# Kernel tuning notes

Measured on AMD Instinct MI355X. Metric: run time of the kernel, lower is better.

The kernel has to match this reference:

```python
import jax, jax.numpy as jnp
import numpy as np

OUTPUT_DIM = 8192
LEAF_DIM = 128
FEAT = 1024
BATCH = 8192
NUM_LEAVES = int(np.ceil(OUTPUT_DIM / LEAF_DIM))          # 64
NUM_INTERNAL = NUM_LEAVES - 1                              # 63
DEPTH = int(np.ceil(np.log2(NUM_LEAVES)))                  # 6


def _build_path_maps():
    # Exactly mirrors the Keras layer's __init__ path-map construction.
    nodes = np.full((NUM_LEAVES, DEPTH), -1, dtype=np.int32)
    dirs_ = np.full((NUM_LEAVES, DEPTH), -1, dtype=np.int32)
    for leaf_idx in range(NUM_LEAVES):
        curr = NUM_INTERNAL + leaf_idx
        path, dirs = [], []
        while curr > 0:
            parent = (curr - 1) // 2
            path.append(parent)
            dirs.append((curr - 1) % 2)
            curr = parent
        n = len(path)
        nodes[leaf_idx, :n] = path[::-1]
        dirs_[leaf_idx, :n] = dirs[::-1]
    return jnp.asarray(nodes), jnp.asarray(dirs_)


def setup_inputs() -> dict:
    key = jax.random.key(0)
    k1, k2, k3 = jax.random.split(key, 3)
    x = jax.random.normal(k1, (BATCH, FEAT), dtype=jnp.float32)
    # glorot-ish scaling for stable softmax / outputs
    routing_weights = jax.random.normal(k2, (NUM_INTERNAL, FEAT, 2), dtype=jnp.float32) * (1.0 / np.sqrt(FEAT))
    leaf_weights = jax.random.normal(k3, (NUM_LEAVES, FEAT, LEAF_DIM), dtype=jnp.float32) * (1.0 / np.sqrt(FEAT))
    leaf_biases = jnp.zeros((NUM_LEAVES, LEAF_DIM), dtype=jnp.float32)
    path_nodes, path_directions = _build_path_maps()
    return {
        "x": x,
        "routing_weights": routing_weights,
        "leaf_weights": leaf_weights,
        "leaf_biases": leaf_biases,
        "path_nodes": path_nodes,
        "path_directions": path_directions,
    }


def reference(x, routing_weights, leaf_weights, leaf_biases, path_nodes, path_directions):
    # 1) Routing probabilities at every internal node: (B, N, 2)
    logits = jnp.einsum("bf,nfd->bnd", x, routing_weights)
    probs = jax.nn.softmax(logits, axis=-1)
    # 2) Path probability per leaf: gather the (node, direction) prob along
    #    each leaf's root-to-leaf path, treating -1 padding as prob 1.
    safe_nodes = jnp.maximum(path_nodes, 0)        # (L, D)
    safe_dirs = jnp.maximum(path_directions, 0)    # (L, D)
    step_probs = probs[:, safe_nodes, safe_dirs]   # (B, L, D)
    step_probs = jnp.where(path_nodes[None, :, :] >= 0, step_probs, 1.0)
    leaf_probs = jnp.prod(step_probs, axis=-1)     # (B, L)
    # 3) Batched per-leaf dense: (B, L, d)
    leaf_outputs = jnp.einsum("bf,lfo->blo", x, leaf_weights) + leaf_biases[None, :, :]
    # 4) Weight and concat ('concat' combination, linear activation)
    weighted = leaf_probs[:, :, None] * leaf_outputs
    return weighted.reshape(x.shape[0], -1)        # (B, L*d)
```

## Files before the change

kernel.cpp:

```cpp
#include <hip/hip_runtime.h>


typedef __attribute__((ext_vector_type(8))) short short8;
typedef __attribute__((ext_vector_type(4))) float f32x4;

#define BATCH 8192
#define FEAT  1024
#define NLEAF 64
#define LEAFD 128
#define OUTD  8192

#define BM 256
#define BN 256
#define BK 64
#define NT (FEAT / BK)

__device__ __forceinline__ unsigned short f2bf(float f) {
    union { float f; unsigned int u; } c; c.f = f;
    unsigned int u = c.u;
    return (unsigned short)((u + 0x7FFFu + ((u >> 16) & 1u)) >> 16);
}

__device__ __forceinline__ void gload16(const void* g, void* l) {
    __builtin_amdgcn_global_load_lds(
        (const __attribute__((address_space(1))) unsigned int*)g,
        (__attribute__((address_space(3))) unsigned int*)l, 16, 0, 0);
}


__global__ __launch_bounds__(256) void cvt_x(const float* __restrict__ x,
                                             unsigned short* __restrict__ xb) {
    const int i = (blockIdx.x * 256 + threadIdx.x) * 4;
    const float4 v = *(const float4*)(x + i);
    ushort4 o;
    o.x = f2bf(v.x); o.y = f2bf(v.y); o.z = f2bf(v.z); o.w = f2bf(v.w);
    *(ushort4*)(xb + i) = o;
}

__global__ __launch_bounds__(256) void cvt_lw(const float* __restrict__ lw,
                                              unsigned short* __restrict__ wt) {
    __shared__ float tile[32][33];
    const int l  = blockIdx.x;
    const int k0 = blockIdx.y * 32;
    const int o0 = blockIdx.z * 32;
    const int tr = threadIdx.x >> 5;
    const int tc = threadIdx.x & 31;
    const float* src = lw + (size_t)l * (FEAT * LEAFD);
#pragma unroll
    for (int p = 0; p < 4; ++p) {
        const int r = p * 8 + tr;
        tile[r][tc] = src[(size_t)(k0 + r) * LEAFD + o0 + tc];
    }
    __syncthreads();
    unsigned short* dst = wt + (size_t)l * (LEAFD * FEAT);
#pragma unroll
    for (int p = 0; p < 4; ++p) {
        const int oo = p * 8 + tr;
        dst[(size_t)(o0 + oo) * FEAT + k0 + tc] = f2bf(tile[tc][oo]);
    }
}

__global__ __launch_bounds__(256) void cvt_rw(const float* __restrict__ rw,
                                              unsigned short* __restrict__ rt) {
    const int gid = blockIdx.x * 256 + threadIdx.x;
    const int row = gid >> 10;
    const int f   = gid & 1023;
    const float v = (row < 126) ? rw[(size_t)(row >> 1) * 2048 + f * 2 + (row & 1)] : 0.0f;
    rt[gid] = f2bf(v);
}

__global__ __launch_bounds__(256) void routing_gemm(
        const unsigned short* __restrict__ xb,
        const unsigned short* __restrict__ rt,
        float* __restrict__ logits) {
    __shared__ __align__(16) unsigned short As[128 * 32];
    __shared__ __align__(16) unsigned short Bs[128 * 32];
    const int t    = threadIdx.x;
    const int row0 = blockIdx.x * 128;
    const int wv = t >> 6, ln = t & 63;
    const int wm = wv >> 1, wn = wv & 1;
    const int quad = ln >> 4, r16 = ln & 15;

    f32x4 acc[4][4];
#pragma unroll
    for (int i = 0; i < 4; ++i)
#pragma unroll
        for (int j = 0; j < 4; ++j) acc[i][j] = (f32x4)0.0f;

    const unsigned short* ag = xb + (size_t)row0 * FEAT;
    const int srow = t >> 2;
    const int scol = (t & 3) * 8;

    for (int k0 = 0; k0 < FEAT; k0 += 32) {
#pragma unroll
        for (int i = 0; i < 2; ++i) {
            gload16(ag + (size_t)(i * 64 + srow) * FEAT + k0 + scol,
                    (char*)As + i * 4096 + t * 16);
            gload16(rt + (size_t)(i * 64 + srow) * FEAT + k0 + scol,
                    (char*)Bs + i * 4096 + t * 16);
        }
        __syncthreads();
        short8 a[4], b[4];
#pragma unroll
        for (int mi = 0; mi < 4; ++mi)
            a[mi] = *(const short8*)&As[(wm * 64 + mi * 16 + r16) * 32 + quad * 8];
#pragma unroll
        for (int ni = 0; ni < 4; ++ni)
            b[ni] = *(const short8*)&Bs[(wn * 64 + ni * 16 + r16) * 32 + quad * 8];
#pragma unroll
        for (int mi = 0; mi < 4; ++mi)
#pragma unroll
            for (int ni = 0; ni < 4; ++ni)
                acc[mi][ni] = __builtin_amdgcn_mfma_f32_16x16x32_bf16(
                    a[mi], b[ni], acc[mi][ni], 0, 0, 0);
        __syncthreads();
    }
#pragma unroll
    for (int mi = 0; mi < 4; ++mi) {
        const int r = wm * 64 + mi * 16 + quad * 4;
#pragma unroll
        for (int ni = 0; ni < 4; ++ni) {
            const int c = wn * 64 + ni * 16 + r16;
#pragma unroll
            for (int reg = 0; reg < 4; ++reg)
                logits[(size_t)(row0 + r + reg) * 128 + c] = acc[mi][ni][reg];
        }
    }
}

__global__ __launch_bounds__(256) void leafprob(
        const float* __restrict__ logits,
        const int* __restrict__ pnodes,
        const int* __restrict__ pdirs,
        float* __restrict__ lp) {
    const int gid  = blockIdx.x * 256 + threadIdx.x;
    const int b    = gid >> 6;
    const int leaf = gid & 63;
    float prod = 1.0f;
#pragma unroll
    for (int d = 0; d < 6; ++d) {
        const int n   = pnodes[leaf * 6 + d];
        const int dir = pdirs[leaf * 6 + d];
        if (n >= 0) {
            const float z0 = logits[(size_t)b * 128 + n * 2];
            const float z1 = logits[(size_t)b * 128 + n * 2 + 1];
            const float zd = dir ? z1 : z0;
            const float zo = dir ? z0 : z1;
            prod *= 1.0f / (1.0f + __expf(zo - zd));
        }
    }
    lp[gid] = prod;
}

__global__ __launch_bounds__(512, 2) void leaf_gemm(
        const unsigned short* __restrict__ xb,
        const unsigned short* __restrict__ wt,
        const float* __restrict__ lp,
        const float* __restrict__ bias,
        float* __restrict__ out) {
    __shared__ __align__(16) char lds[134144];
    char* Abuf = lds;
    char* Bbuf = lds + 65536;
    float* lps = (float*)(lds + 131072);
    float* bs  = (float*)(lds + 133120);

    const int t = threadIdx.x;

    const int wg  = blockIdx.x;
    const int swz = (wg & 7) * 128 + (wg >> 3);
    const int by  = swz >> 5;
    const int bx  = swz & 31;
    const int row0 = bx * BM;
    const int col0 = by * BN;
    const int l0   = by * 2;

    {
        const int j = t >> 8, r = t & 255;
        lps[j * 256 + r] = lp[(size_t)(row0 + r) * NLEAF + l0 + j];
        if (t < 256) bs[t] = bias[l0 * LEAFD + t];
    }
    asm volatile("s_waitcnt vmcnt(0)" ::: "memory");

    int goff0, goff1;
    {
#pragma unroll
        for (int i = 0; i < 2; ++i) {
            const int q   = t + i * 512;
            const int sub = q >> 6;
            const int qq  = q & 63;
            const int r   = qq >> 2;
            const int cc  = (qq & 3) * 8;
            const int row = (sub >> 1) * 16 + r;
            const int col = (sub & 1) * 32 + (cc ^ ((r & 8) ? 16 : 0));
            const int off = row * FEAT + col;
            if (i == 0) goff0 = off; else goff1 = off;
        }
    }

    const unsigned short* Ag = xb + (size_t)row0 * FEAT;
    const unsigned short* Bg = wt + (size_t)col0 * FEAT;

#define STAGE(gbase, ldsbase, bufsel, h, kt)                                   \
    do {                                                                       \
        gload16(gbase + (h) * 131072 + (kt) * BK + goff0,                      \
                (ldsbase) + (bufsel) * 32768 + (h) * 16384 + t * 16);          \
        gload16(gbase + (h) * 131072 + (kt) * BK + goff1,                      \
                (ldsbase) + (bufsel) * 32768 + (h) * 16384 + 8192 + t * 16);   \
    } while (0)

    const int wv   = t >> 6;
    const int ln   = t & 63;
    const int wm   = wv >> 2;
    const int wn   = wv & 3;
    const int quad = ln >> 4;
    const int r16  = ln & 15;

    const int fb = r16 * 64 + ((quad * 8) ^ ((r16 & 8) << 1)) * 2;
    const char* Afb = Abuf + wm * 16384 + fb;
    const char* Bfb = Bbuf + wn * 8192 + fb;

    f32x4 acc[8][4];
#pragma unroll
    for (int i = 0; i < 8; ++i)
#pragma unroll
        for (int j = 0; j < 4; ++j) acc[i][j] = (f32x4)0.0f;

    STAGE(Bg, Bbuf, 0, 0, 0);
    STAGE(Bg, Bbuf, 0, 1, 0);
    STAGE(Ag, Abuf, 0, 0, 0);
    STAGE(Ag, Abuf, 0, 1, 0);
    STAGE(Bg, Bbuf, 1, 0, 1);
    STAGE(Bg, Bbuf, 1, 1, 1);
    asm volatile("s_waitcnt vmcnt(4)" ::: "memory");
    __builtin_amdgcn_s_barrier();

    short8 a[4][2], b01[2][2], b23[2][2];

#pragma unroll 2
    for (int kt = 0; kt < NT; ++kt) {
        const int cur = kt & 1;
        const char* Ac = Afb + cur * 32768;
        const char* Bc = Bfb + cur * 32768;

#pragma unroll
        for (int ni = 0; ni < 2; ++ni)
#pragma unroll
            for (int ks = 0; ks < 2; ++ks) {
                b01[ni][ks] = *(const short8*)(Bc + ni * 2048 + ks * 1024);
                b23[ni][ks] = *(const short8*)(Bc + (ni + 2) * 2048 + ks * 1024);
            }
#pragma unroll
        for (int mi = 0; mi < 4; ++mi)
#pragma unroll
            for (int ks = 0; ks < 2; ++ks)
                a[mi][ks] = *(const short8*)(Ac + mi * 2048 + ks * 1024);
        if (kt + 1 < NT) STAGE(Ag, Abuf, (kt + 1) & 1, 0, kt + 1);
        __builtin_amdgcn_s_setprio(1);
#pragma unroll
        for (int mi = 0; mi < 4; ++mi)
#pragma unroll
            for (int ni = 0; ni < 2; ++ni)
#pragma unroll
                for (int ks = 0; ks < 2; ++ks)
                    acc[mi][ni] = __builtin_amdgcn_mfma_f32_16x16x32_bf16(
                        a[mi][ks], b01[ni][ks], acc[mi][ni], 0, 0, 0);
        __builtin_amdgcn_s_setprio(0);
        asm volatile("s_waitcnt lgkmcnt(0)" ::: "memory");
        __builtin_amdgcn_s_barrier();

        if (kt + 1 < NT) STAGE(Ag, Abuf, (kt + 1) & 1, 1, kt + 1);
        if (kt + 2 < NT) STAGE(Bg, Bbuf, kt & 1, 0, kt + 2);
        __builtin_amdgcn_s_setprio(1);
#pragma unroll
        for (int mi = 0; mi < 4; ++mi)
#pragma unroll
            for (int ni = 0; ni < 2; ++ni)
#pragma unroll
                for (int ks = 0; ks < 2; ++ks)
                    acc[mi][ni + 2] = __builtin_amdgcn_mfma_f32_16x16x32_bf16(
                        a[mi][ks], b23[ni][ks], acc[mi][ni + 2], 0, 0, 0);
        __builtin_amdgcn_s_setprio(0);
#pragma unroll
        for (int mi = 0; mi < 4; ++mi)
#pragma unroll
            for (int ks = 0; ks < 2; ++ks)
                a[mi][ks] = *(const short8*)(Ac + (mi + 4) * 2048 + ks * 1024);
        if (kt + 2 < NT) STAGE(Bg, Bbuf, kt & 1, 1, kt + 2);
        asm volatile("s_waitcnt lgkmcnt(0)" ::: "memory");
        __builtin_amdgcn_s_setprio(1);
#pragma unroll
        for (int mi = 0; mi < 4; ++mi)
#pragma unroll
            for (int ni = 0; ni < 2; ++ni)
#pragma unroll
                for (int ks = 0; ks < 2; ++ks)
                    acc[mi + 4][ni] = __builtin_amdgcn_mfma_f32_16x16x32_bf16(
                        a[mi][ks], b01[ni][ks], acc[mi + 4][ni], 0, 0, 0);
#pragma unroll
        for (int mi = 0; mi < 4; ++mi)
#pragma unroll
            for (int ni = 0; ni < 2; ++ni)
#pragma unroll
                for (int ks = 0; ks < 2; ++ks)
                    acc[mi + 4][ni + 2] = __builtin_amdgcn_mfma_f32_16x16x32_bf16(
                        a[mi][ks], b23[ni][ks], acc[mi + 4][ni + 2], 0, 0, 0);
        __builtin_amdgcn_s_setprio(0);

        if (kt + 2 < NT) {
            asm volatile("s_waitcnt vmcnt(4)" ::: "memory");
        } else if (kt + 1 < NT) {
            asm volatile("s_waitcnt vmcnt(0)" ::: "memory");
        }
        __builtin_amdgcn_s_barrier();
    }
#undef STAGE

    const float* lpw = lps + (wn >> 1) * 256;
#pragma unroll
    for (int mi = 0; mi < 8; ++mi) {
        const int r = wm * 128 + mi * 16 + quad * 4;
#pragma unroll
        for (int ni = 0; ni < 4; ++ni) {
            const int c  = wn * 64 + ni * 16 + r16;
            const float bv = bs[c];
#pragma unroll
            for (int reg = 0; reg < 4; ++reg) {
                const float v = (acc[mi][ni][reg] + bv) * lpw[r + reg];
                __builtin_nontemporal_store(
                    v, &out[(size_t)(row0 + r + reg) * OUTD + col0 + c]);
            }
        }
    }
}


extern "C" void kernel_launch(void* const* d_in, const int* in_sizes, int n_in,
                              void* d_out, int out_size, void* d_ws, size_t ws_size,
                              hipStream_t stream) {
    const float* x    = (const float*)d_in[0];
    const float* rw   = (const float*)d_in[1];
    const float* lw   = (const float*)d_in[2];
    const float* bias = (const float*)d_in[3];
    const int*   pn   = (const int*)d_in[4];
    const int*   pd   = (const int*)d_in[5];
    float* out = (float*)d_out;

    char* ws = (char*)d_ws;
    unsigned short* xb     = (unsigned short*)(ws);
    unsigned short* wt     = (unsigned short*)(ws + 16777216);
    unsigned short* rt     = (unsigned short*)(ws + 33554432);
    float*          logits = (float*)(ws + 33816576);
    float*          lpv    = (float*)(ws + 38010880);

    cvt_x<<<8192, 256, 0, stream>>>(x, xb);
    cvt_lw<<<dim3(64, 32, 4), 256, 0, stream>>>(lw, wt);
    cvt_rw<<<512, 256, 0, stream>>>(rw, rt);
    routing_gemm<<<64, 256, 0, stream>>>(xb, rt, logits);
    leafprob<<<2048, 256, 0, stream>>>(logits, pn, pd, lpv);
    leaf_gemm<<<dim3(1024), 512, 0, stream>>>(xb, wt, lpv, bias, out);
}
```

Measured before the change: 513.5 us.

## Fuse leaf-probability computation into routing GEMM and restage leaf GEMM loads

Merges the routing GEMM and the leaf-probability kernel: logits are kept in shared memory and path products are computed in the same block, which removes a kernel launch and the logits round trip through global memory. In the leaf GEMM, both halves of the next A tile are now issued before the first MFMA phase rather than split across phases, and the epilogue loop is reordered so each thread writes one output row across ni. The fused kernel uses about 66KB of LDS with only 64 blocks, and the changed load staging alters how memory traffic overlaps with compute.

```diff
diff --git a/kernel.cpp b/kernel.cpp
--- a/kernel.cpp
+++ b/kernel.cpp
@@ -69,18 +69,26 @@
     rt[gid] = f2bf(v);
 }
 
-__global__ __launch_bounds__(256) void routing_gemm(
+__global__ __launch_bounds__(256) void routing_lp(
         const unsigned short* __restrict__ xb,
         const unsigned short* __restrict__ rt,
-        float* __restrict__ logits) {
+        const int* __restrict__ pn,
+        const int* __restrict__ pd,
+        float* __restrict__ lp) {
     __shared__ __align__(16) unsigned short As[128 * 32];
     __shared__ __align__(16) unsigned short Bs[128 * 32];
+    __shared__ float lg[128][130];
+    __shared__ int pnl[NLEAF * 6], pdl[NLEAF * 6];
+
     const int t    = threadIdx.x;
     const int row0 = blockIdx.x * 128;
     const int wv = t >> 6, ln = t & 63;
     const int wm = wv >> 1, wn = wv & 1;
     const int quad = ln >> 4, r16 = ln & 15;
 
+    if (t < NLEAF * 6) { pnl[t] = pn[t]; pdl[t] = pd[t]; }
+    if (t + 256 < NLEAF * 6) { pnl[t + 256] = pn[t + 256]; pdl[t + 256] = pd[t + 256]; }
+
     f32x4 acc[4][4];
 #pragma unroll
     for (int i = 0; i < 4; ++i)
@@ -123,33 +131,30 @@
             const int c = wn * 64 + ni * 16 + r16;
 #pragma unroll
             for (int reg = 0; reg < 4; ++reg)
-                logits[(size_t)(row0 + r + reg) * 128 + c] = acc[mi][ni][reg];
-        }
-    }
-}
-
-__global__ __launch_bounds__(256) void leafprob(
-        const float* __restrict__ logits,
-        const int* __restrict__ pnodes,
-        const int* __restrict__ pdirs,
-        float* __restrict__ lp) {
-    const int gid  = blockIdx.x * 256 + threadIdx.x;
-    const int b    = gid >> 6;
-    const int leaf = gid & 63;
-    float prod = 1.0f;
-#pragma unroll
-    for (int d = 0; d < 6; ++d) {
-        const int n   = pnodes[leaf * 6 + d];
-        const int dir = pdirs[leaf * 6 + d];
-        if (n >= 0) {
-            const float z0 = logits[(size_t)b * 128 + n * 2];
-            const float z1 = logits[(size_t)b * 128 + n * 2 + 1];
-            const float zd = dir ? z1 : z0;
-            const float zo = dir ? z0 : z1;
-            prod *= 1.0f / (1.0f + __expf(zo - zd));
-        }
-    }
-    lp[gid] = prod;
+                lg[r + reg][c] = acc[mi][ni][reg];
+        }
+    }
+    __syncthreads();
+#pragma unroll 4
+    for (int i = 0; i < 32; ++i) {
+        const int idx  = i * 256 + t;
+        const int b    = idx >> 6;
+        const int leaf = idx & 63;
+        float prod = 1.0f;
+#pragma unroll
+        for (int d = 0; d < 6; ++d) {
+            const int n   = pnl[leaf * 6 + d];
+            const int dir = pdl[leaf * 6 + d];
+            if (n >= 0) {
+                const float z0 = lg[b][n * 2];
+                const float z1 = lg[b][n * 2 + 1];
+                const float zd = dir ? z1 : z0;
+                const float zo = dir ? z0 : z1;
+                prod *= 1.0f / (1.0f + __expf(zo - zd));
+            }
+        }
+        lp[(size_t)(row0 + b) * NLEAF + leaf] = prod;
+    }
 }
 
 __global__ __launch_bounds__(512, 2) void leaf_gemm(
@@ -254,7 +259,10 @@
 #pragma unroll
             for (int ks = 0; ks < 2; ++ks)
                 a[mi][ks] = *(const short8*)(Ac + mi * 2048 + ks * 1024);
-        if (kt + 1 < NT) STAGE(Ag, Abuf, (kt + 1) & 1, 0, kt + 1);
+        if (kt + 1 < NT) {
+            STAGE(Ag, Abuf, (kt + 1) & 1, 0, kt + 1);
+            STAGE(Ag, Abuf, (kt + 1) & 1, 1, kt + 1);
+        }
         __builtin_amdgcn_s_setprio(1);
 #pragma unroll
         for (int mi = 0; mi < 4; ++mi)
@@ -268,7 +276,6 @@
         asm volatile("s_waitcnt lgkmcnt(0)" ::: "memory");
         __builtin_amdgcn_s_barrier();
 
-        if (kt + 1 < NT) STAGE(Ag, Abuf, (kt + 1) & 1, 1, kt + 1);
         if (kt + 2 < NT) STAGE(Bg, Bbuf, kt & 1, 0, kt + 2);
         __builtin_amdgcn_s_setprio(1);
 #pragma unroll
@@ -320,14 +327,14 @@
     for (int mi = 0; mi < 8; ++mi) {
         const int r = wm * 128 + mi * 16 + quad * 4;
 #pragma unroll
-        for (int ni = 0; ni < 4; ++ni) {
-            const int c  = wn * 64 + ni * 16 + r16;
-            const float bv = bs[c];
-#pragma unroll
-            for (int reg = 0; reg < 4; ++reg) {
-                const float v = (acc[mi][ni][reg] + bv) * lpw[r + reg];
-                __builtin_nontemporal_store(
-                    v, &out[(size_t)(row0 + r + reg) * OUTD + col0 + c]);
+        for (int reg = 0; reg < 4; ++reg) {
+            const float lv = lpw[r + reg];
+            float* orow = out + (size_t)(row0 + r + reg) * OUTD + col0 + wn * 64;
+#pragma unroll
+            for (int ni = 0; ni < 4; ++ni) {
+                const int c = ni * 16 + r16;
+                const float v = (acc[mi][ni][reg] + bs[wn * 64 + c]) * lv;
+                __builtin_nontemporal_store(v, orow + c);
             }
         }
     }
@@ -346,16 +353,14 @@
     float* out = (float*)d_out;
 
     char* ws = (char*)d_ws;
-    unsigned short* xb     = (unsigned short*)(ws);
-    unsigned short* wt     = (unsigned short*)(ws + 16777216);
-    unsigned short* rt     = (unsigned short*)(ws + 33554432);
-    float*          logits = (float*)(ws + 33816576);
-    float*          lpv    = (float*)(ws + 38010880);
+    unsigned short* xb  = (unsigned short*)(ws);
+    unsigned short* wt  = (unsigned short*)(ws + 16777216);
+    unsigned short* rt  = (unsigned short*)(ws + 33554432);
+    float*          lpv = (float*)(ws + 38010880);
 
     cvt_x<<<8192, 256, 0, stream>>>(x, xb);
     cvt_lw<<<dim3(64, 32, 4), 256, 0, stream>>>(lw, wt);
     cvt_rw<<<512, 256, 0, stream>>>(rw, rt);
-    routing_gemm<<<64, 256, 0, stream>>>(xb, rt, logits);
-    leafprob<<<2048, 256, 0, stream>>>(logits, pn, pd, lpv);
-    leaf_gemm<<<dim3(1024), 512, 0, stream>>>(xb, wt, lpv, bias, out);
-}
+    routing_lp<<<64, 256, 0, stream>>>(xb, rt, pn, pd, lpv);
+    leaf_gemm<<<1024, 512, 0, stream>>>(xb, wt, lpv, bias, out);
+}
```

Result: slower. 525.6 us (+2.4%).
